# Kernel tuning notes

Hardware: AMD Instinct MI355X
Metric: run time of the kernel (lower is better)

The kernel has to match this reference:

```python
import jax, jax.numpy as jnp
import numpy as np
import math

B, L, E, H, D = 2, 2048, 2048, 16, 128
LOGIT_SCALE_MAX = math.log(1.0 / 0.01)
EPS = 1e-6


def rms_norm(x, scale, eps=EPS):
    # UIOLayerNorm: no mean subtraction, no bias, fp32 internals
    x32 = x.astype(jnp.float32)
    ms = jnp.mean(x32 * x32, axis=-1, keepdims=True)
    return (scale * (x32 * jax.lax.rsqrt(ms + eps)).astype(x.dtype)).astype(x.dtype)


def apply_rotary(x, rope):
    # x: [b, l, h, d]; rope: [b, l, d] interpreted as (cos, sin) interleaved pairs
    b, l, h, d = x.shape
    xr = x.astype(jnp.float32).reshape(b, l, h, d // 2, 2)
    rc = rope.astype(jnp.float32).reshape(b, l, 1, d // 2, 2)
    out = jnp.stack(
        [xr[..., 0] * rc[..., 0] - xr[..., 1] * rc[..., 1],
         xr[..., 1] * rc[..., 0] + xr[..., 0] * rc[..., 1]], axis=-1)
    return out.reshape(b, l, h, d).astype(x.dtype)


def l2_normalize(x, eps=1e-12):
    # matches F.normalize(dim=-1): x / max(||x||, eps)
    n = jnp.sqrt(jnp.sum(x * x, axis=-1, keepdims=True))
    return x / jnp.maximum(n, eps)


def setup_inputs() -> dict:
    key = jax.random.key(0)
    ks = jax.random.split(key, 12)
    scale = 1.0 / math.sqrt(E)
    return {
        "inputs_q": jax.random.normal(ks[0], (B, L, E), jnp.float32),
        "inputs_kv": jax.random.normal(ks[1], (B, L, E), jnp.float32),
        "bias": jax.random.normal(ks[2], (1, 1, L, L), jnp.float32),
        "q_sinusoids": jax.random.uniform(ks[3], (B, L, D), jnp.float32, -1.0, 1.0),
        "k_sinusoids": jax.random.uniform(ks[4], (B, L, D), jnp.float32, -1.0, 1.0),
        "Wq": jax.random.normal(ks[5], (E, E), jnp.float32) * scale,
        "Wk": jax.random.normal(ks[6], (E, E), jnp.float32) * scale,
        "Wv": jax.random.normal(ks[7], (E, E), jnp.float32) * scale,
        "Wo": jax.random.normal(ks[8], (E, E), jnp.float32) * scale,
        "q_norm_scale": jnp.ones((D,), jnp.float32),
        "k_norm_scale": jnp.ones((D,), jnp.float32),
        "logit_scale": jnp.full((H,), math.log(10.0), jnp.float32),
    }


def reference(inputs_q, inputs_kv, bias, q_sinusoids, k_sinusoids,
              Wq, Wk, Wv, Wo, q_norm_scale, k_norm_scale, logit_scale):
    dtype = inputs_q.dtype
    b, ql, e = inputs_q.shape
    kl = inputs_kv.shape[1]
    # QKV projections (nn.Linear, no bias), split heads -> [b, len, h, d]
    q = (inputs_q @ Wq.T).reshape(b, ql, H, D)
    k = (inputs_kv @ Wk.T).reshape(b, kl, H, D)
    v = (inputs_kv @ Wv.T).reshape(b, kl, H, D)
    # qk_norm (UIO RMS norm over head_dim)
    q = rms_norm(q, q_norm_scale)
    k = rms_norm(k, k_norm_scale)
    # RoPE
    q = apply_rotary(q, q_sinusoids)
    k = apply_rotary(k, k_sinusoids)
    # float32_logits
    q32 = q.astype(jnp.float32)
    k32 = k.astype(jnp.float32)
    # scaled cosine attention: L2-normalize q,k; learned per-head logit scale
    scores = jnp.einsum("bqhd,bkhd->bhqk", l2_normalize(q32), l2_normalize(k32))
    ls = jnp.exp(jnp.minimum(logit_scale, LOGIT_SCALE_MAX))
    scores = scores * ls[None, :, None, None]
    scores = scores + bias.astype(scores.dtype)
    attn = jax.nn.softmax(scores, axis=-1).astype(dtype)
    out = jnp.einsum("bhqk,bkhd->bqhd", attn, v)
    out = out.reshape(b, ql, e)
    return out @ Wo.T
```

## Files before the change

kernel.cpp:

```cpp
#include <hip/hip_runtime.h>
#include <hip/hip_bf16.h>

#define B_ 2
#define L_ 2048
#define E_ 2048
#define H_ 16
#define D_ 128
#define M_ (B_*L_)
#define LOGIT_SCALE_MAX_ 4.6051701859880914f
#define LOG2E_ 1.44269504088896f

typedef __bf16 bf16_t;
typedef __bf16 bf16x2 __attribute__((ext_vector_type(2)));
typedef __bf16 bf16x4 __attribute__((ext_vector_type(4)));
typedef __bf16 bf16x8 __attribute__((ext_vector_type(8)));
typedef float f32x4 __attribute__((ext_vector_type(4)));
typedef float f32x16 __attribute__((ext_vector_type(16)));

#define KSB(p, r, cb) ((p) * 32768 + (r) * 256 + ((cb) ^ (((r) & 7) << 4)))
#define VSB(p, r, cb) ((p) * 32768 + 16384 + (r) * 128 + ((cb) ^ (((r) & 7) << 4)))

#define NW_ 4194304L
#define NX_ 8388608L

__global__ void cvt_all_k(const float* __restrict__ xq, const float* __restrict__ xkv,
                          const float* __restrict__ bias,
                          const float* __restrict__ wq, const float* __restrict__ wk,
                          const float* __restrict__ wv, const float* __restrict__ wo,
                          bf16_t* __restrict__ ws) {
    const long NW4 = NW_ / 4, NX4 = NX_ / 4;
    long i4 = (long)blockIdx.x * 256 + threadIdx.x;
    const float* src; long off; float scale = 1.0f;
    if (i4 < 4 * NW4) {
        long r = i4 / NW4;
        src = (r == 0) ? wq : (r == 1) ? wk : (r == 2) ? wv : wo;
        off = i4 - r * NW4;
    } else if (i4 < 5 * NW4) {
        src = bias; off = i4 - 4 * NW4; scale = LOG2E_;
    } else if (i4 < 5 * NW4 + NX4) {
        src = xq; off = i4 - 5 * NW4;
    } else {
        src = xkv; off = i4 - 5 * NW4 - NX4;
    }
    float4 v = ((const float4*)src)[off];
    bf16x4 o = { (bf16_t)(v.x * scale), (bf16_t)(v.y * scale),
                 (bf16_t)(v.z * scale), (bf16_t)(v.w * scale) };
    ((bf16x4*)ws)[i4] = o;
}

template<typename OutT, int GROUPS>
__global__ __launch_bounds__(512, 2) void gemm256(
    const bf16_t* __restrict__ A0g, const bf16_t* __restrict__ A1g,
    const bf16_t* __restrict__ W0, OutT* __restrict__ C0) {
    __shared__ __align__(16) unsigned char smem[131072];
    const int tid = threadIdx.x;
    const int wid = tid >> 6, lane = tid & 63;
    const int fr = lane & 15, fq = lane >> 4;
    const int wm = wid >> 2, wn = wid & 3;
    int bid = blockIdx.x;
    { int cpx = (int)gridDim.x >> 3; bid = (bid & 7) * cpx + (bid >> 3); }
    const int g = (GROUPS > 1) ? (bid >> 7) : 0;
    const int wg = (GROUPS > 1) ? (bid & 127) : bid;
    const int bm = wg >> 3, bn = wg & 7;
    const long arow0 = (long)bm * 256;
    const long brow0 = (long)bn * 256;
    const bf16_t* Ab = ((GROUPS > 1 && g > 0) ? A1g : A0g) + arow0 * E_;
    const bf16_t* Wb = W0 + (long)g * (long)E_ * E_ + brow0 * E_;

    f32x4 acc[8][4] = {};

    const int srow = tid >> 2;
    const int sc16 = tid & 3;
    auto STG = [&](const bf16_t* base, unsigned matOff, int h, unsigned bufb, int kt) {
        #pragma unroll
        for (int kk = 0; kk < 2; ++kk) {
            int col = kk * 32 + ((sc16 ^ ((srow >> 1) & 3)) * 8);
            __builtin_amdgcn_global_load_lds(
                (const __attribute__((address_space(1))) void*)(base + (long)(h * 128 + srow) * E_ + kt + col),
                (__attribute__((address_space(3))) void*)(smem + bufb + matOff + h * 16384u + kk * 8192u + tid * 16), 16, 0, 0);
        }
    };
    auto LDA = [&](unsigned pb, int kk, int mi) -> bf16x8 {
        int r = wm * 128 + mi * 16 + fr;
        int lr = r & 127;
        return *(const bf16x8*)(smem + pb + (unsigned)(r >> 7) * 16384u + kk * 8192u + lr * 64 + ((fq ^ ((lr >> 1) & 3)) << 4));
    };
    auto LDB = [&](unsigned pb, int kk, int ni) -> bf16x8 {
        int r = wn * 64 + ni * 16 + fr;
        int lr = r & 127;
        return *(const bf16x8*)(smem + pb + 32768u + (unsigned)(r >> 7) * 16384u + kk * 8192u + lr * 64 + ((fq ^ ((lr >> 1) & 3)) << 4));
    };

    STG(Ab, 0u,     0, 0u, 0); STG(Ab, 0u,     1, 0u, 0);
    STG(Wb, 32768u, 0, 0u, 0); STG(Wb, 32768u, 1, 0u, 0);
    STG(Wb, 32768u, 0, 65536u, 64); STG(Wb, 32768u, 1, 65536u, 64);
    asm volatile("s_waitcnt vmcnt(4)" ::: "memory");
    __builtin_amdgcn_s_barrier();

    bf16x8 bq[2][4];
    #pragma unroll 2
    for (int t = 0; t < 32; ++t) {
        const unsigned pb = (unsigned)(t & 1) * 65536u;
        const unsigned sbA = 65536u - pb;
        const int ktA = ((t + 1) & 31) * 64;
        const int ktB = ((t + 2) & 31) * 64;
        bf16x8 a[2][2];
        #pragma unroll
        for (int kk = 0; kk < 2; ++kk) {
            a[kk][0] = LDA(pb, kk, 0); a[kk][1] = LDA(pb, kk, 1);
            #pragma unroll
            for (int ni = 0; ni < 4; ++ni) bq[kk][ni] = LDB(pb, kk, ni);
        }
        STG(Ab, 0u, 0, sbA, ktA);
        __builtin_amdgcn_s_barrier();
        asm volatile("s_waitcnt lgkmcnt(0)" ::: "memory");
        __builtin_amdgcn_sched_barrier(0);
        __builtin_amdgcn_s_setprio(1);
        #pragma unroll
        for (int kk = 0; kk < 2; ++kk)
            #pragma unroll
            for (int ni = 0; ni < 4; ++ni) {
                acc[0][ni] = __builtin_amdgcn_mfma_f32_16x16x32_bf16(a[kk][0], bq[kk][ni], acc[0][ni], 0, 0, 0);
                acc[1][ni] = __builtin_amdgcn_mfma_f32_16x16x32_bf16(a[kk][1], bq[kk][ni], acc[1][ni], 0, 0, 0);
            }
        __builtin_amdgcn_s_setprio(0);
        __builtin_amdgcn_s_barrier();
        #pragma unroll
        for (int kk = 0; kk < 2; ++kk) { a[kk][0] = LDA(pb, kk, 2); a[kk][1] = LDA(pb, kk, 3); }
        STG(Ab, 0u, 1, sbA, ktA);
        __builtin_amdgcn_s_barrier();
        asm volatile("s_waitcnt lgkmcnt(0)" ::: "memory");
        __builtin_amdgcn_sched_barrier(0);
        __builtin_amdgcn_s_setprio(1);
        #pragma unroll
        for (int kk = 0; kk < 2; ++kk)
            #pragma unroll
            for (int ni = 0; ni < 4; ++ni) {
                acc[2][ni] = __builtin_amdgcn_mfma_f32_16x16x32_bf16(a[kk][0], bq[kk][ni], acc[2][ni], 0, 0, 0);
                acc[3][ni] = __builtin_amdgcn_mfma_f32_16x16x32_bf16(a[kk][1], bq[kk][ni], acc[3][ni], 0, 0, 0);
            }
        __builtin_amdgcn_s_setprio(0);
        __builtin_amdgcn_s_barrier();
        #pragma unroll
        for (int kk = 0; kk < 2; ++kk) { a[kk][0] = LDA(pb, kk, 4); a[kk][1] = LDA(pb, kk, 5); }
        STG(Wb, 32768u, 0, pb, ktB);
        __builtin_amdgcn_s_barrier();
        asm volatile("s_waitcnt lgkmcnt(0)" ::: "memory");
        __builtin_amdgcn_sched_barrier(0);
        __builtin_amdgcn_s_setprio(1);
        #pragma unroll
        for (int kk = 0; kk < 2; ++kk)
            #pragma unroll
            for (int ni = 0; ni < 4; ++ni) {
                acc[4][ni] = __builtin_amdgcn_mfma_f32_16x16x32_bf16(a[kk][0], bq[kk][ni], acc[4][ni], 0, 0, 0);
                acc[5][ni] = __builtin_amdgcn_mfma_f32_16x16x32_bf16(a[kk][1], bq[kk][ni], acc[5][ni], 0, 0, 0);
            }
        __builtin_amdgcn_s_setprio(0);
        __builtin_amdgcn_s_barrier();
        #pragma unroll
        for (int kk = 0; kk < 2; ++kk) { a[kk][0] = LDA(pb, kk, 6); a[kk][1] = LDA(pb, kk, 7); }
        STG(Wb, 32768u, 1, pb, ktB);
        asm volatile("s_waitcnt vmcnt(4)" ::: "memory");
        __builtin_amdgcn_s_barrier();
        asm volatile("s_waitcnt lgkmcnt(0)" ::: "memory");
        __builtin_amdgcn_sched_barrier(0);
        __builtin_amdgcn_s_setprio(1);
        #pragma unroll
        for (int kk = 0; kk < 2; ++kk)
            #pragma unroll
            for (int ni = 0; ni < 4; ++ni) {
                acc[6][ni] = __builtin_amdgcn_mfma_f32_16x16x32_bf16(a[kk][0], bq[kk][ni], acc[6][ni], 0, 0, 0);
                acc[7][ni] = __builtin_amdgcn_mfma_f32_16x16x32_bf16(a[kk][1], bq[kk][ni], acc[7][ni], 0, 0, 0);
            }
        __builtin_amdgcn_s_setprio(0);
        __builtin_amdgcn_s_barrier();
    }
    asm volatile("s_waitcnt vmcnt(0)" ::: "memory");
    OutT* Cg = C0 + (long)g * M_ * E_;
    #pragma unroll
    for (int mi = 0; mi < 8; ++mi) {
        #pragma unroll
        for (int i = 0; i < 4; ++i) {
            long row = arow0 + wm * 128 + mi * 16 + fq * 4 + i;
            OutT* crow = Cg + row * E_ + brow0 + wn * 64 + fr;
            #pragma unroll
            for (int ni = 0; ni < 4; ++ni)
                crow[ni * 16] = (OutT)acc[mi][ni][i];
        }
    }
}

template<typename OutT>
__global__ __launch_bounds__(512, 2) void gemm8o(
    const bf16_t* __restrict__ A0g, const bf16_t* __restrict__ W0, OutT* __restrict__ C0) {
    __shared__ __align__(16) unsigned char smem[98304];
    const int tid = threadIdx.x;
    const int wid = tid >> 6, lane = tid & 63;
    const int fr = lane & 15, fq = lane >> 4;
    const int wm = wid & 3, wn = wid >> 2;
    int bid = blockIdx.x;
    { int cpx = (int)gridDim.x >> 3; bid = (bid & 7) * cpx + (bid >> 3); }
    const int bm = bid >> 4, bn = bid & 15;
    const long arow0 = (long)bm * 256;
    const long brow0 = (long)bn * 128;
    const bf16_t* Ab = A0g + arow0 * E_;
    const bf16_t* Wb = W0 + brow0 * E_;

    f32x4 acc[4][4] = {};

    auto STAGE_A = [&](unsigned sbase, int kk, int j, int ktn_) {
        int row = j * 128 + (tid >> 2);
        int c16 = tid & 3;
        int col = kk * 32 + ((c16 ^ ((row >> 1) & 3)) * 8);
        __builtin_amdgcn_global_load_lds(
            (const __attribute__((address_space(1))) void*)(Ab + (long)row * E_ + ktn_ + col),
            (__attribute__((address_space(3))) void*)(smem + sbase + kk * 16384 + j * 8192 + tid * 16), 16, 0, 0);
    };
    auto STAGE_B = [&](unsigned sbase, int kk, int ktn_) {
        int row = tid >> 2;
        int c16 = tid & 3;
        int col = kk * 32 + ((c16 ^ ((row >> 1) & 3)) * 8);
        __builtin_amdgcn_global_load_lds(
            (const __attribute__((address_space(1))) void*)(Wb + (long)row * E_ + ktn_ + col),
            (__attribute__((address_space(3))) void*)(smem + sbase + 32768 + kk * 8192 + tid * 16), 16, 0, 0);
    };
    auto LDA = [&](unsigned pbase, int kk, int mi) -> bf16x8 {
        int row = wm * 64 + mi * 16 + fr;
        return *(const bf16x8*)(smem + pbase + kk * 16384 + row * 64 + ((fq ^ ((row >> 1) & 3)) << 4));
    };
    auto LDB = [&](unsigned pbase, int kk, int ni) -> bf16x8 {
        int row = wn * 64 + ni * 16 + fr;
        return *(const bf16x8*)(smem + pbase + 32768 + kk * 8192 + row * 64 + ((fq ^ ((row >> 1) & 3)) << 4));
    };

    STAGE_A(0, 0, 0, 0); STAGE_A(0, 0, 1, 0); STAGE_B(0, 0, 0);
    STAGE_A(0, 1, 0, 0); STAGE_A(0, 1, 1, 0); STAGE_B(0, 1, 0);
    asm volatile("s_waitcnt vmcnt(0)" ::: "memory");
    __builtin_amdgcn_s_barrier();

    #pragma unroll 2
    for (int t = 0; t < 32; ++t) {
        const unsigned pb = (unsigned)(t & 1) * 49152u;
        const unsigned sb = 49152u - pb;
        const int ktn = (t < 31) ? (t + 1) * 64 : 0;
        bf16x8 bq[4], a0, a1;
        a0 = LDA(pb, 0, 0); a1 = LDA(pb, 0, 1);
        bq[0] = LDB(pb, 0, 0); bq[1] = LDB(pb, 0, 1); bq[2] = LDB(pb, 0, 2); bq[3] = LDB(pb, 0, 3);
        STAGE_A(sb, 0, 0, ktn); STAGE_A(sb, 0, 1, ktn);
        __builtin_amdgcn_s_barrier();
        asm volatile("s_waitcnt lgkmcnt(0)" ::: "memory");
        __builtin_amdgcn_sched_barrier(0);
        __builtin_amdgcn_s_setprio(1);
        #pragma unroll
        for (int ni = 0; ni < 4; ++ni) {
            acc[0][ni] = __builtin_amdgcn_mfma_f32_16x16x32_bf16(a0, bq[ni], acc[0][ni], 0, 0, 0);
            acc[1][ni] = __builtin_amdgcn_mfma_f32_16x16x32_bf16(a1, bq[ni], acc[1][ni], 0, 0, 0);
        }
        __builtin_amdgcn_s_setprio(0);
        __builtin_amdgcn_s_barrier();
        a0 = LDA(pb, 0, 2); a1 = LDA(pb, 0, 3);
        STAGE_B(sb, 0, ktn);
        asm volatile("s_waitcnt vmcnt(3)" ::: "memory");
        __builtin_amdgcn_s_barrier();
        asm volatile("s_waitcnt lgkmcnt(0)" ::: "memory");
        __builtin_amdgcn_sched_barrier(0);
        __builtin_amdgcn_s_setprio(1);
        #pragma unroll
        for (int ni = 0; ni < 4; ++ni) {
            acc[2][ni] = __builtin_amdgcn_mfma_f32_16x16x32_bf16(a0, bq[ni], acc[2][ni], 0, 0, 0);
            acc[3][ni] = __builtin_amdgcn_mfma_f32_16x16x32_bf16(a1, bq[ni], acc[3][ni], 0, 0, 0);
        }
        __builtin_amdgcn_s_setprio(0);
        __builtin_amdgcn_s_barrier();
        a0 = LDA(pb, 1, 0); a1 = LDA(pb, 1, 1);
        bq[0] = LDB(pb, 1, 0); bq[1] = LDB(pb, 1, 1); bq[2] = LDB(pb, 1, 2); bq[3] = LDB(pb, 1, 3);
        STAGE_A(sb, 1, 0, ktn); STAGE_A(sb, 1, 1, ktn);
        __builtin_amdgcn_s_barrier();
        asm volatile("s_waitcnt lgkmcnt(0)" ::: "memory");
        __builtin_amdgcn_sched_barrier(0);
        __builtin_amdgcn_s_setprio(1);
        #pragma unroll
        for (int ni = 0; ni < 4; ++ni) {
            acc[0][ni] = __builtin_amdgcn_mfma_f32_16x16x32_bf16(a0, bq[ni], acc[0][ni], 0, 0, 0);
            acc[1][ni] = __builtin_amdgcn_mfma_f32_16x16x32_bf16(a1, bq[ni], acc[1][ni], 0, 0, 0);
        }
        __builtin_amdgcn_s_setprio(0);
        __builtin_amdgcn_s_barrier();
        a0 = LDA(pb, 1, 2); a1 = LDA(pb, 1, 3);
        STAGE_B(sb, 1, ktn);
        asm volatile("s_waitcnt vmcnt(3)" ::: "memory");
        __builtin_amdgcn_s_barrier();
        asm volatile("s_waitcnt lgkmcnt(0)" ::: "memory");
        __builtin_amdgcn_sched_barrier(0);
        __builtin_amdgcn_s_setprio(1);
        #pragma unroll
        for (int ni = 0; ni < 4; ++ni) {
            acc[2][ni] = __builtin_amdgcn_mfma_f32_16x16x32_bf16(a0, bq[ni], acc[2][ni], 0, 0, 0);
            acc[3][ni] = __builtin_amdgcn_mfma_f32_16x16x32_bf16(a1, bq[ni], acc[3][ni], 0, 0, 0);
        }
        __builtin_amdgcn_s_setprio(0);
        __builtin_amdgcn_s_barrier();
    }
    #pragma unroll
    for (int mi = 0; mi < 4; ++mi) {
        #pragma unroll
        for (int i = 0; i < 4; ++i) {
            long row = arow0 + wm * 64 + mi * 16 + fq * 4 + i;
            OutT* crow = C0 + row * E_ + brow0 + wn * 64 + fr;
            #pragma unroll
            for (int ni = 0; ni < 4; ++ni)
                crow[ni * 16] = (OutT)acc[mi][ni][i];
        }
    }
}

__global__ __launch_bounds__(256) void post_tv_k(
    const bf16_t* __restrict__ Pq, const bf16_t* __restrict__ Pk,
    const bf16_t* __restrict__ Vp,
    const float* __restrict__ qsins, const float* __restrict__ ksins,
    const float* __restrict__ qnscale, const float* __restrict__ knscale,
    bf16_t* __restrict__ outq, bf16_t* __restrict__ outk, bf16_t* __restrict__ Vt) {
    __shared__ bf16_t t[64 * 64];
    if (blockIdx.x < 32768) {
        const int wid = threadIdx.x >> 6, lane = threadIdx.x & 63;
        const int half = blockIdx.x >> 14;
        const long g = (long)(blockIdx.x & 16383) * 4 + wid;
        const bf16_t* P = half ? Pk : Pq;
        const float* sins = half ? ksins : qsins;
        const float* nscale = half ? knscale : qnscale;
        bf16_t* out = half ? outk : outq;
        const int h = (int)(g % H_);
        const long bl = g / H_;
        const int b = (int)(bl / L_), l = (int)(bl % L_);
        bf16x2 xv = *(const bf16x2*)(P + g * D_ + lane * 2);
        float x0 = (float)xv[0], x1 = (float)xv[1];
        float ss = x0 * x0 + x1 * x1;
        #pragma unroll
        for (int m = 1; m < 64; m <<= 1) ss += __shfl_xor(ss, m);
        float r = rsqrtf(ss * (1.0f / 128.0f) + 1e-6f);
        float y0 = x0 * r * nscale[lane * 2];
        float y1 = x1 * r * nscale[lane * 2 + 1];
        float2 cs = *(const float2*)(sins + bl * D_ + lane * 2);
        float z0 = y0 * cs.x - y1 * cs.y;
        float z1 = y1 * cs.x + y0 * cs.y;
        float n2 = z0 * z0 + z1 * z1;
        #pragma unroll
        for (int m = 1; m < 64; m <<= 1) n2 += __shfl_xor(n2, m);
        float inv = 1.0f / fmaxf(sqrtf(n2), 1e-12f);
        bf16x2 o = { (bf16_t)(z0 * inv), (bf16_t)(z1 * inv) };
        *(bf16x2*)(out + (((long)b * H_ + h) * L_ + l) * D_ + lane * 2) = o;
    } else {
        const int idx = blockIdx.x - 32768;
        const int lb = idx & 31;
        const int db = (idx >> 5) & 1;
        const int bh = idx >> 6;
        const int b = bh >> 4, h = bh & 15;
        const bf16_t* src = Vp + ((long)(b * L_ + lb * 64) * H_ + h) * D_ + db * 64;
        #pragma unroll
        for (int it = 0; it < 2; ++it) {
            int i = it * 256 + threadIdx.x;
            int r = i >> 3, c8 = i & 7;
            bf16x8 v = *(const bf16x8*)(src + (long)r * H_ * D_ + c8 * 8);
            *(bf16x8*)&t[r * 64 + (c8 ^ (r >> 3)) * 8] = v;
        }
        __syncthreads();
        bf16_t* dst = Vt + ((long)(b * H_ + h) * D_ + db * 64) * L_ + lb * 64;
        #pragma unroll
        for (int it = 0; it < 2; ++it) {
            int i = it * 256 + threadIdx.x;
            int d = i >> 3, l8 = i & 7;
            bf16x8 o;
            #pragma unroll
            for (int j = 0; j < 8; ++j) {
                int l = l8 * 8 + j;
                o[j] = t[l * 64 + ((d >> 3) ^ l8) * 8 + (d & 7)];
            }
            *(bf16x8*)(dst + (long)d * L_ + l8 * 8) = o;
        }
    }
}

__global__ __launch_bounds__(256, 2) void attn_k(
    const bf16_t* __restrict__ Qn, const bf16_t* __restrict__ Kn,
    const bf16_t* __restrict__ Vt, const bf16_t* __restrict__ biasb,
    const float* __restrict__ lsg, bf16_t* __restrict__ AO) {
    __shared__ __align__(16) unsigned char smem[65536];
    const int tid = threadIdx.x;
    const int w = tid >> 6, lane = tid & 63;
    const int lane31 = lane & 31, hi = lane >> 5;
    const int qb = blockIdx.x, bh = blockIdx.y;
    const int b = bh >> 4, h = bh & 15;
    const float lsc2 = __expf(fminf(lsg[h], LOGIT_SCALE_MAX_)) * LOG2E_;
    const int qr0 = qb * 128;
    const int qloc = w * 32 + lane31;
    const bf16_t* qrow  = Qn + (((long)b * H_ + h) * L_ + qr0 + qloc) * D_;
    const bf16_t* kbase = Kn + (((long)b * H_ + h) * L_) * D_;
    const bf16_t* vtbase = Vt + ((long)(b * H_ + h) * D_) * L_;
    const bf16_t* brow  = biasb + (long)(qr0 + qloc) * L_;

    const int ksr = tid >> 4, ksc = (tid & 15) * 8;
    const int vsr = tid >> 3, vsc = (tid & 7) * 8;

    bf16x8 qreg[8];
    #pragma unroll
    for (int kk = 0; kk < 8; ++kk)
        qreg[kk] = *(const bf16x8*)(qrow + kk * 16 + 8 * hi);

    f32x16 oacc[4] = {};
    float l_ = 0.f;

    bf16x8 kreg[4], vreg[4];
    #pragma unroll
    for (int it = 0; it < 4; ++it) {
        kreg[it] = *(const bf16x8*)(kbase + (long)(it * 16 + ksr) * D_ + ksc);
        vreg[it] = *(const bf16x8*)(vtbase + (long)(it * 32 + vsr) * L_ + vsc);
    }
    #pragma unroll
    for (int it = 0; it < 4; ++it) {
        *(bf16x8*)(smem + KSB(0, it * 16 + ksr, ksc * 2)) = kreg[it];
        *(bf16x8*)(smem + VSB(0, it * 32 + vsr, vsc * 2)) = vreg[it];
    }
    int p = 0;

    for (int kt = 0; kt < L_; kt += 64) {
        __syncthreads();
        const int ktn = (kt + 64 < L_) ? kt + 64 : 0;
        #pragma unroll
        for (int it = 0; it < 4; ++it) {
            kreg[it] = *(const bf16x8*)(kbase + (long)(ktn + it * 16 + ksr) * D_ + ksc);
            vreg[it] = *(const bf16x8*)(vtbase + (long)(it * 32 + vsr) * L_ + ktn + vsc);
        }
        bf16x4 bb[2][4];
        #pragma unroll
        for (int f = 0; f < 2; ++f)
            #pragma unroll
            for (int rr = 0; rr < 4; ++rr)
                bb[f][rr] = *(const bf16x4*)(brow + kt + f * 32 + rr * 8 + 4 * hi);
        f32x16 sacc[2] = {};
        __builtin_amdgcn_s_setprio(1);
        #pragma unroll
        for (int kk = 0; kk < 8; ++kk) {
            bf16x8 ak0 = *(const bf16x8*)(smem + KSB(p, lane31,      kk * 32 + 16 * hi));
            bf16x8 ak1 = *(const bf16x8*)(smem + KSB(p, 32 + lane31, kk * 32 + 16 * hi));
            sacc[0] = __builtin_amdgcn_mfma_f32_32x32x16_bf16(ak0, qreg[kk], sacc[0], 0, 0, 0);
            sacc[1] = __builtin_amdgcn_mfma_f32_32x32x16_bf16(ak1, qreg[kk], sacc[1], 0, 0, 0);
        }
        __builtin_amdgcn_s_setprio(0);
        float ps = 0.f;
        unsigned int wv[2][4][2];
        #pragma unroll
        for (int f = 0; f < 2; ++f)
            #pragma unroll
            for (int rr = 0; rr < 4; ++rr)
                #pragma unroll
                for (int wi = 0; wi < 2; ++wi) {
                    float pa = __builtin_amdgcn_exp2f(sacc[f][rr * 4 + wi * 2]     * lsc2 + (float)bb[f][rr][wi * 2]);
                    float pc = __builtin_amdgcn_exp2f(sacc[f][rr * 4 + wi * 2 + 1] * lsc2 + (float)bb[f][rr][wi * 2 + 1]);
                    ps += pa + pc;
                    bf16x2 t = { (bf16_t)pa, (bf16_t)pc };
                    wv[f][rr][wi] = __builtin_bit_cast(unsigned int, t);
                }
        ps += __shfl_xor(ps, 32);
        l_ += ps;
        bf16x8 pb_[4];
        #pragma unroll
        for (int kk = 0; kk < 4; ++kk) {
            const int f = kk >> 1;
            const int a2 = (kk & 1) * 2;
            unsigned int A0 = wv[f][a2][0],     A1 = wv[f][a2][1];
            unsigned int B0 = wv[f][a2 + 1][0], B1 = wv[f][a2 + 1][1];
            unsigned int own0  = hi ? B0 : A0;
            unsigned int own1  = hi ? B1 : A1;
            unsigned int send0 = hi ? A0 : B0;
            unsigned int send1 = hi ? A1 : B1;
            unsigned int recv0 = __shfl_xor(send0, 32);
            unsigned int recv1 = __shfl_xor(send1, 32);
            uint4 uu;
            uu.x = hi ? recv0 : own0;
            uu.y = hi ? recv1 : own1;
            uu.z = hi ? own0  : recv0;
            uu.w = hi ? own1  : recv1;
            pb_[kk] = __builtin_bit_cast(bf16x8, uu);
        }
        __builtin_amdgcn_s_setprio(1);
        #pragma unroll
        for (int df = 0; df < 4; ++df)
            #pragma unroll
            for (int kk = 0; kk < 4; ++kk) {
                bf16x8 av = *(const bf16x8*)(smem + VSB(p, df * 32 + lane31, kk * 32 + 16 * hi));
                oacc[df] = __builtin_amdgcn_mfma_f32_32x32x16_bf16(av, pb_[kk], oacc[df], 0, 0, 0);
            }
        __builtin_amdgcn_s_setprio(0);
        if (kt + 64 < L_) {
            #pragma unroll
            for (int it = 0; it < 4; ++it) {
                *(bf16x8*)(smem + KSB(p ^ 1, it * 16 + ksr, ksc * 2)) = kreg[it];
                *(bf16x8*)(smem + VSB(p ^ 1, it * 32 + vsr, vsc * 2)) = vreg[it];
            }
        }
        p ^= 1;
    }
    __syncthreads();
    float inv = 1.0f / l_;
    #pragma unroll
    for (int df = 0; df < 4; ++df)
        #pragma unroll
        for (int rg = 0; rg < 16; ++rg) {
            int d = df * 32 + (rg & 3) + 8 * (rg >> 2) + 4 * hi;
            *(bf16_t*)(smem + qloc * 264 + d * 2) = (bf16_t)(oacc[df][rg] * inv);
        }
    __syncthreads();
    #pragma unroll
    for (int it = 0; it < 8; ++it) {
        int idx = it * 256 + tid;
        int row = idx >> 4, c = idx & 15;
        bf16x8 v = *(const bf16x8*)(smem + row * 264 + c * 16);
        *(bf16x8*)(AO + ((long)b * L_ + qr0 + row) * E_ + h * D_ + c * 8) = v;
    }
}

extern "C" void kernel_launch(void* const* d_in, const int* in_sizes, int n_in,
                              void* d_out, int out_size, void* d_ws, size_t ws_size,
                              hipStream_t stream) {
    const float* inputs_q  = (const float*)d_in[0];
    const float* inputs_kv = (const float*)d_in[1];
    const float* bias      = (const float*)d_in[2];
    const float* q_sin     = (const float*)d_in[3];
    const float* k_sin     = (const float*)d_in[4];
    const float* Wq        = (const float*)d_in[5];
    const float* Wk        = (const float*)d_in[6];
    const float* Wv        = (const float*)d_in[7];
    const float* Wo        = (const float*)d_in[8];
    const float* qns       = (const float*)d_in[9];
    const float* kns       = (const float*)d_in[10];
    const float* lsg       = (const float*)d_in[11];

    bf16_t* ws = (bf16_t*)d_ws;
    const long NW = NW_;
    const long NX = NX_;
    bf16_t* Wq_b   = ws;
    bf16_t* Wo_b   = ws + 3 * NW;
    bf16_t* bias_b = ws + 4 * NW;
    bf16_t* Xq     = bias_b + NW;
    bf16_t* Xkv    = Xq + NX;
    bf16_t* Qp     = Xkv + NX;
    bf16_t* Kp     = Qp + NX;
    bf16_t* Vp     = Kp + NX;
    bf16_t* Qn = Xq;
    bf16_t* Kn = Xkv;
    bf16_t* AO = Qp;
    bf16_t* Vtr = Kp;
    if (ws_size < (size_t)(5 * NW + 5 * NX) * 2) return;

    {
        long n4 = (5 * NW + 2 * NX) / 4;
        cvt_all_k<<<dim3((unsigned)(n4 / 256)), dim3(256), 0, stream>>>(
            inputs_q, inputs_kv, bias, Wq, Wk, Wv, Wo, ws);
    }

    gemm256<bf16_t, 3><<<dim3(384), dim3(512), 0, stream>>>(Xq, Xkv, Wq_b, Qp);

    post_tv_k<<<dim3(34816), dim3(256), 0, stream>>>(
        Qp, Kp, Vp, q_sin, k_sin, qns, kns, Qn, Kn, Vtr);

    attn_k<<<dim3(L_ / 128, B_ * H_), dim3(256), 0, stream>>>(Qn, Kn, Vtr, bias_b, lsg, AO);

    gemm8o<float><<<dim3(256), dim3(512), 0, stream>>>(AO, Wo_b, (float*)d_out);
}
```

Measured before the change: 311.1 us.

## Split QKV GEMM into mixed full and half-height tiles to balance waves

The QKV projection GEMM now launches 512 blocks. The first 256 compute full 256x256 tiles, and the last 128 tiles are split into two 128-row halves each, so the 256-CU device gets a better-balanced second wave instead of a partial one. The output projection GEMM reuses the half-tile path of the same kernel in place of the separate gemm8o kernel, so it now uses 128x256 tiles rather than 256x128. Half tiles reuse the W tile less per block, which adds global and L2 traffic.

```diff
diff --git a/kernel.cpp b/kernel.cpp
--- a/kernel.cpp
+++ b/kernel.cpp
@@ -48,8 +48,8 @@
     ((bf16x4*)ws)[i4] = o;
 }
 
-template<typename OutT, int GROUPS>
-__global__ __launch_bounds__(512, 2) void gemm256(
+template<typename OutT, int GROUPS, int FULLB>
+__global__ __launch_bounds__(512, 2) void gemm_mix(
     const bf16_t* __restrict__ A0g, const bf16_t* __restrict__ A1g,
     const bf16_t* __restrict__ W0, OutT* __restrict__ C0) {
     __shared__ __align__(16) unsigned char smem[131072];
@@ -57,20 +57,29 @@
     const int wid = tid >> 6, lane = tid & 63;
     const int fr = lane & 15, fq = lane >> 4;
     const int wm = wid >> 2, wn = wid & 3;
-    int bid = blockIdx.x;
-    { int cpx = (int)gridDim.x >> 3; bid = (bid & 7) * cpx + (bid >> 3); }
-    const int g = (GROUPS > 1) ? (bid >> 7) : 0;
-    const int wg = (GROUPS > 1) ? (bid & 127) : bid;
-    const int bm = wg >> 3, bn = wg & 7;
-    const long arow0 = (long)bm * 256;
+    int slot, hsel, isfull;
+    {
+        int bid = blockIdx.x;
+        if (FULLB > 0 && bid < FULLB) {
+            slot = (bid & 7) * (FULLB >> 3) + (bid >> 3);
+            hsel = 0; isfull = 1;
+        } else {
+            const int n = (int)gridDim.x - FULLB;
+            int sub = bid - FULLB;
+            int s = (sub & 7) * (n >> 3) + (sub >> 3);
+            slot = FULLB + (s >> 1); hsel = s & 1; isfull = 0;
+        }
+    }
+    const int g = slot >> 7;
+    const int r0 = slot & 127;
+    const int bm = r0 >> 3, bn = r0 & 7;
+    const long arow0 = (long)bm * 256 + (long)hsel * 128;
     const long brow0 = (long)bn * 256;
     const bf16_t* Ab = ((GROUPS > 1 && g > 0) ? A1g : A0g) + arow0 * E_;
     const bf16_t* Wb = W0 + (long)g * (long)E_ * E_ + brow0 * E_;
-
-    f32x4 acc[8][4] = {};
-
     const int srow = tid >> 2;
     const int sc16 = tid & 3;
+
     auto STG = [&](const bf16_t* base, unsigned matOff, int h, unsigned bufb, int kt) {
         #pragma unroll
         for (int kk = 0; kk < 2; ++kk) {
@@ -80,8 +89,7 @@
                 (__attribute__((address_space(3))) void*)(smem + bufb + matOff + h * 16384u + kk * 8192u + tid * 16), 16, 0, 0);
         }
     };
-    auto LDA = [&](unsigned pb, int kk, int mi) -> bf16x8 {
-        int r = wm * 128 + mi * 16 + fr;
+    auto LDA = [&](unsigned pb, int kk, int r) -> bf16x8 {
         int lr = r & 127;
         return *(const bf16x8*)(smem + pb + (unsigned)(r >> 7) * 16384u + kk * 8192u + lr * 64 + ((fq ^ ((lr >> 1) & 3)) << 4));
     };
@@ -91,226 +99,201 @@
         return *(const bf16x8*)(smem + pb + 32768u + (unsigned)(r >> 7) * 16384u + kk * 8192u + lr * 64 + ((fq ^ ((lr >> 1) & 3)) << 4));
     };
 
-    STG(Ab, 0u,     0, 0u, 0); STG(Ab, 0u,     1, 0u, 0);
-    STG(Wb, 32768u, 0, 0u, 0); STG(Wb, 32768u, 1, 0u, 0);
-    STG(Wb, 32768u, 0, 65536u, 64); STG(Wb, 32768u, 1, 65536u, 64);
-    asm volatile("s_waitcnt vmcnt(4)" ::: "memory");
-    __builtin_amdgcn_s_barrier();
-
-    bf16x8 bq[2][4];
-    #pragma unroll 2
-    for (int t = 0; t < 32; ++t) {
-        const unsigned pb = (unsigned)(t & 1) * 65536u;
-        const unsigned sbA = 65536u - pb;
-        const int ktA = ((t + 1) & 31) * 64;
-        const int ktB = ((t + 2) & 31) * 64;
-        bf16x8 a[2][2];
-        #pragma unroll
-        for (int kk = 0; kk < 2; ++kk) {
-            a[kk][0] = LDA(pb, kk, 0); a[kk][1] = LDA(pb, kk, 1);
-            #pragma unroll
-            for (int ni = 0; ni < 4; ++ni) bq[kk][ni] = LDB(pb, kk, ni);
-        }
-        STG(Ab, 0u, 0, sbA, ktA);
-        __builtin_amdgcn_s_barrier();
-        asm volatile("s_waitcnt lgkmcnt(0)" ::: "memory");
-        __builtin_amdgcn_sched_barrier(0);
-        __builtin_amdgcn_s_setprio(1);
-        #pragma unroll
-        for (int kk = 0; kk < 2; ++kk)
-            #pragma unroll
-            for (int ni = 0; ni < 4; ++ni) {
-                acc[0][ni] = __builtin_amdgcn_mfma_f32_16x16x32_bf16(a[kk][0], bq[kk][ni], acc[0][ni], 0, 0, 0);
-                acc[1][ni] = __builtin_amdgcn_mfma_f32_16x16x32_bf16(a[kk][1], bq[kk][ni], acc[1][ni], 0, 0, 0);
-            }
-        __builtin_amdgcn_s_setprio(0);
-        __builtin_amdgcn_s_barrier();
-        #pragma unroll
-        for (int kk = 0; kk < 2; ++kk) { a[kk][0] = LDA(pb, kk, 2); a[kk][1] = LDA(pb, kk, 3); }
-        STG(Ab, 0u, 1, sbA, ktA);
-        __builtin_amdgcn_s_barrier();
-        asm volatile("s_waitcnt lgkmcnt(0)" ::: "memory");
-        __builtin_amdgcn_sched_barrier(0);
-        __builtin_amdgcn_s_setprio(1);
-        #pragma unroll
-        for (int kk = 0; kk < 2; ++kk)
-            #pragma unroll
-            for (int ni = 0; ni < 4; ++ni) {
-                acc[2][ni] = __builtin_amdgcn_mfma_f32_16x16x32_bf16(a[kk][0], bq[kk][ni], acc[2][ni], 0, 0, 0);
-                acc[3][ni] = __builtin_amdgcn_mfma_f32_16x16x32_bf16(a[kk][1], bq[kk][ni], acc[3][ni], 0, 0, 0);
-            }
-        __builtin_amdgcn_s_setprio(0);
-        __builtin_amdgcn_s_barrier();
-        #pragma unroll
-        for (int kk = 0; kk < 2; ++kk) { a[kk][0] = LDA(pb, kk, 4); a[kk][1] = LDA(pb, kk, 5); }
-        STG(Wb, 32768u, 0, pb, ktB);
-        __builtin_amdgcn_s_barrier();
-        asm volatile("s_waitcnt lgkmcnt(0)" ::: "memory");
-        __builtin_amdgcn_sched_barrier(0);
-        __builtin_amdgcn_s_setprio(1);
-        #pragma unroll
-        for (int kk = 0; kk < 2; ++kk)
-            #pragma unroll
-            for (int ni = 0; ni < 4; ++ni) {
-                acc[4][ni] = __builtin_amdgcn_mfma_f32_16x16x32_bf16(a[kk][0], bq[kk][ni], acc[4][ni], 0, 0, 0);
-                acc[5][ni] = __builtin_amdgcn_mfma_f32_16x16x32_bf16(a[kk][1], bq[kk][ni], acc[5][ni], 0, 0, 0);
-            }
-        __builtin_amdgcn_s_setprio(0);
-        __builtin_amdgcn_s_barrier();
-        #pragma unroll
-        for (int kk = 0; kk < 2; ++kk) { a[kk][0] = LDA(pb, kk, 6); a[kk][1] = LDA(pb, kk, 7); }
-        STG(Wb, 32768u, 1, pb, ktB);
+    if (FULLB > 0 && isfull) {
+        f32x4 acc[8][4] = {};
+        STG(Ab, 0u,     0, 0u, 0); STG(Ab, 0u,     1, 0u, 0);
+        STG(Wb, 32768u, 0, 0u, 0); STG(Wb, 32768u, 1, 0u, 0);
+        STG(Wb, 32768u, 0, 65536u, 64); STG(Wb, 32768u, 1, 65536u, 64);
         asm volatile("s_waitcnt vmcnt(4)" ::: "memory");
         __builtin_amdgcn_s_barrier();
-        asm volatile("s_waitcnt lgkmcnt(0)" ::: "memory");
-        __builtin_amdgcn_sched_barrier(0);
-        __builtin_amdgcn_s_setprio(1);
-        #pragma unroll
-        for (int kk = 0; kk < 2; ++kk)
-            #pragma unroll
-            for (int ni = 0; ni < 4; ++ni) {
-                acc[6][ni] = __builtin_amdgcn_mfma_f32_16x16x32_bf16(a[kk][0], bq[kk][ni], acc[6][ni], 0, 0, 0);
-                acc[7][ni] = __builtin_amdgcn_mfma_f32_16x16x32_bf16(a[kk][1], bq[kk][ni], acc[7][ni], 0, 0, 0);
-            }
-        __builtin_amdgcn_s_setprio(0);
+        bf16x8 bq[2][4];
+        #pragma unroll 2
+        for (int t = 0; t < 32; ++t) {
+            const unsigned pb = (unsigned)(t & 1) * 65536u;
+            const unsigned sbA = 65536u - pb;
+            const int ktA = ((t + 1) & 31) * 64;
+            const int ktB = ((t + 2) & 31) * 64;
+            bf16x8 a[2][2];
+            #pragma unroll
+            for (int kk = 0; kk < 2; ++kk) {
+                a[kk][0] = LDA(pb, kk, wm * 128 + 0 * 16 + fr);
+                a[kk][1] = LDA(pb, kk, wm * 128 + 1 * 16 + fr);
+                #pragma unroll
+                for (int ni = 0; ni < 4; ++ni) bq[kk][ni] = LDB(pb, kk, ni);
+            }
+            STG(Ab, 0u, 0, sbA, ktA);
+            __builtin_amdgcn_s_barrier();
+            asm volatile("s_waitcnt lgkmcnt(0)" ::: "memory");
+            __builtin_amdgcn_sched_barrier(0);
+            __builtin_amdgcn_s_setprio(1);
+            #pragma unroll
+            for (int kk = 0; kk < 2; ++kk)
+                #pragma unroll
+                for (int ni = 0; ni < 4; ++ni) {
+                    acc[0][ni] = __builtin_amdgcn_mfma_f32_16x16x32_bf16(a[kk][0], bq[kk][ni], acc[0][ni], 0, 0, 0);
+                    acc[1][ni] = __builtin_amdgcn_mfma_f32_16x16x32_bf16(a[kk][1], bq[kk][ni], acc[1][ni], 0, 0, 0);
+                }
+            __builtin_amdgcn_s_setprio(0);
+            __builtin_amdgcn_s_barrier();
+            #pragma unroll
+            for (int kk = 0; kk < 2; ++kk) {
+                a[kk][0] = LDA(pb, kk, wm * 128 + 2 * 16 + fr);
+                a[kk][1] = LDA(pb, kk, wm * 128 + 3 * 16 + fr);
+            }
+            STG(Ab, 0u, 1, sbA, ktA);
+            __builtin_amdgcn_s_barrier();
+            asm volatile("s_waitcnt lgkmcnt(0)" ::: "memory");
+            __builtin_amdgcn_sched_barrier(0);
+            __builtin_amdgcn_s_setprio(1);
+            #pragma unroll
+            for (int kk = 0; kk < 2; ++kk)
+                #pragma unroll
+                for (int ni = 0; ni < 4; ++ni) {
+                    acc[2][ni] = __builtin_amdgcn_mfma_f32_16x16x32_bf16(a[kk][0], bq[kk][ni], acc[2][ni], 0, 0, 0);
+                    acc[3][ni] = __builtin_amdgcn_mfma_f32_16x16x32_bf16(a[kk][1], bq[kk][ni], acc[3][ni], 0, 0, 0);
+                }
+            __builtin_amdgcn_s_setprio(0);
+            __builtin_amdgcn_s_barrier();
+            #pragma unroll
+            for (int kk = 0; kk < 2; ++kk) {
+                a[kk][0] = LDA(pb, kk, wm * 128 + 4 * 16 + fr);
+                a[kk][1] = LDA(pb, kk, wm * 128 + 5 * 16 + fr);
+            }
+            STG(Wb, 32768u, 0, pb, ktB);
+            __builtin_amdgcn_s_barrier();
+            asm volatile("s_waitcnt lgkmcnt(0)" ::: "memory");
+            __builtin_amdgcn_sched_barrier(0);
+            __builtin_amdgcn_s_setprio(1);
+            #pragma unroll
+            for (int kk = 0; kk < 2; ++kk)
+                #pragma unroll
+                for (int ni = 0; ni < 4; ++ni) {
+                    acc[4][ni] = __builtin_amdgcn_mfma_f32_16x16x32_bf16(a[kk][0], bq[kk][ni], acc[4][ni], 0, 0, 0);
+                    acc[5][ni] = __builtin_amdgcn_mfma_f32_16x16x32_bf16(a[kk][1], bq[kk][ni], acc[5][ni], 0, 0, 0);
+                }
+            __builtin_amdgcn_s_setprio(0);
+            __builtin_amdgcn_s_barrier();
+            #pragma unroll
+            for (int kk = 0; kk < 2; ++kk) {
+                a[kk][0] = LDA(pb, kk, wm * 128 + 6 * 16 + fr);
+                a[kk][1] = LDA(pb, kk, wm * 128 + 7 * 16 + fr);
+            }
+            STG(Wb, 32768u, 1, pb, ktB);
+            asm volatile("s_waitcnt vmcnt(4)" ::: "memory");
+            __builtin_amdgcn_s_barrier();
+            asm volatile("s_waitcnt lgkmcnt(0)" ::: "memory");
+            __builtin_amdgcn_sched_barrier(0);
+            __builtin_amdgcn_s_setprio(1);
+            #pragma unroll
+            for (int kk = 0; kk < 2; ++kk)
+                #pragma unroll
+                for (int ni = 0; ni < 4; ++ni) {
+                    acc[6][ni] = __builtin_amdgcn_mfma_f32_16x16x32_bf16(a[kk][0], bq[kk][ni], acc[6][ni], 0, 0, 0);
+                    acc[7][ni] = __builtin_amdgcn_mfma_f32_16x16x32_bf16(a[kk][1], bq[kk][ni], acc[7][ni], 0, 0, 0);
+                }
+            __builtin_amdgcn_s_setprio(0);
+            __builtin_amdgcn_s_barrier();
+        }
+        asm volatile("s_waitcnt vmcnt(0)" ::: "memory");
+        OutT* Cg = C0 + (long)g * M_ * E_;
+        #pragma unroll
+        for (int mi = 0; mi < 8; ++mi)
+            #pragma unroll
+            for (int i = 0; i < 4; ++i) {
+                long row = arow0 + wm * 128 + mi * 16 + fq * 4 + i;
+                OutT* crow = Cg + row * E_ + brow0 + wn * 64 + fr;
+                #pragma unroll
+                for (int ni = 0; ni < 4; ++ni)
+                    crow[ni * 16] = (OutT)acc[mi][ni][i];
+            }
+    } else {
+        f32x4 acc[4][4] = {};
+        STG(Ab, 0u,     0, 0u, 0);
+        STG(Wb, 32768u, 0, 0u, 0); STG(Wb, 32768u, 1, 0u, 0);
+        STG(Wb, 32768u, 0, 65536u, 64); STG(Wb, 32768u, 1, 65536u, 64);
+        asm volatile("s_waitcnt vmcnt(4)" ::: "memory");
         __builtin_amdgcn_s_barrier();
-    }
-    asm volatile("s_waitcnt vmcnt(0)" ::: "memory");
-    OutT* Cg = C0 + (long)g * M_ * E_;
-    #pragma unroll
-    for (int mi = 0; mi < 8; ++mi) {
-        #pragma unroll
-        for (int i = 0; i < 4; ++i) {
-            long row = arow0 + wm * 128 + mi * 16 + fq * 4 + i;
-            OutT* crow = Cg + row * E_ + brow0 + wn * 64 + fr;
-            #pragma unroll
-            for (int ni = 0; ni < 4; ++ni)
-                crow[ni * 16] = (OutT)acc[mi][ni][i];
-        }
-    }
-}
-
-template<typename OutT>
-__global__ __launch_bounds__(512, 2) void gemm8o(
-    const bf16_t* __restrict__ A0g, const bf16_t* __restrict__ W0, OutT* __restrict__ C0) {
-    __shared__ __align__(16) unsigned char smem[98304];
-    const int tid = threadIdx.x;
-    const int wid = tid >> 6, lane = tid & 63;
-    const int fr = lane & 15, fq = lane >> 4;
-    const int wm = wid & 3, wn = wid >> 2;
-    int bid = blockIdx.x;
-    { int cpx = (int)gridDim.x >> 3; bid = (bid & 7) * cpx + (bid >> 3); }
-    const int bm = bid >> 4, bn = bid & 15;
-    const long arow0 = (long)bm * 256;
-    const long brow0 = (long)bn * 128;
-    const bf16_t* Ab = A0g + arow0 * E_;
-    const bf16_t* Wb = W0 + brow0 * E_;
-
-    f32x4 acc[4][4] = {};
-
-    auto STAGE_A = [&](unsigned sbase, int kk, int j, int ktn_) {
-        int row = j * 128 + (tid >> 2);
-        int c16 = tid & 3;
-        int col = kk * 32 + ((c16 ^ ((row >> 1) & 3)) * 8);
-        __builtin_amdgcn_global_load_lds(
-            (const __attribute__((address_space(1))) void*)(Ab + (long)row * E_ + ktn_ + col),
-            (__attribute__((address_space(3))) void*)(smem + sbase + kk * 16384 + j * 8192 + tid * 16), 16, 0, 0);
-    };
-    auto STAGE_B = [&](unsigned sbase, int kk, int ktn_) {
-        int row = tid >> 2;
-        int c16 = tid & 3;
-        int col = kk * 32 + ((c16 ^ ((row >> 1) & 3)) * 8);
-        __builtin_amdgcn_global_load_lds(
-            (const __attribute__((address_space(1))) void*)(Wb + (long)row * E_ + ktn_ + col),
-            (__attribute__((address_space(3))) void*)(smem + sbase + 32768 + kk * 8192 + tid * 16), 16, 0, 0);
-    };
-    auto LDA = [&](unsigned pbase, int kk, int mi) -> bf16x8 {
-        int row = wm * 64 + mi * 16 + fr;
-        return *(const bf16x8*)(smem + pbase + kk * 16384 + row * 64 + ((fq ^ ((row >> 1) & 3)) << 4));
-    };
-    auto LDB = [&](unsigned pbase, int kk, int ni) -> bf16x8 {
-        int row = wn * 64 + ni * 16 + fr;
-        return *(const bf16x8*)(smem + pbase + 32768 + kk * 8192 + row * 64 + ((fq ^ ((row >> 1) & 3)) << 4));
-    };
-
-    STAGE_A(0, 0, 0, 0); STAGE_A(0, 0, 1, 0); STAGE_B(0, 0, 0);
-    STAGE_A(0, 1, 0, 0); STAGE_A(0, 1, 1, 0); STAGE_B(0, 1, 0);
-    asm volatile("s_waitcnt vmcnt(0)" ::: "memory");
-    __builtin_amdgcn_s_barrier();
-
-    #pragma unroll 2
-    for (int t = 0; t < 32; ++t) {
-        const unsigned pb = (unsigned)(t & 1) * 49152u;
-        const unsigned sb = 49152u - pb;
-        const int ktn = (t < 31) ? (t + 1) * 64 : 0;
-        bf16x8 bq[4], a0, a1;
-        a0 = LDA(pb, 0, 0); a1 = LDA(pb, 0, 1);
-        bq[0] = LDB(pb, 0, 0); bq[1] = LDB(pb, 0, 1); bq[2] = LDB(pb, 0, 2); bq[3] = LDB(pb, 0, 3);
-        STAGE_A(sb, 0, 0, ktn); STAGE_A(sb, 0, 1, ktn);
-        __builtin_amdgcn_s_barrier();
-        asm volatile("s_waitcnt lgkmcnt(0)" ::: "memory");
-        __builtin_amdgcn_sched_barrier(0);
-        __builtin_amdgcn_s_setprio(1);
-        #pragma unroll
-        for (int ni = 0; ni < 4; ++ni) {
-            acc[0][ni] = __builtin_amdgcn_mfma_f32_16x16x32_bf16(a0, bq[ni], acc[0][ni], 0, 0, 0);
-            acc[1][ni] = __builtin_amdgcn_mfma_f32_16x16x32_bf16(a1, bq[ni], acc[1][ni], 0, 0, 0);
-        }
-        __builtin_amdgcn_s_setprio(0);
-        __builtin_amdgcn_s_barrier();
-        a0 = LDA(pb, 0, 2); a1 = LDA(pb, 0, 3);
-        STAGE_B(sb, 0, ktn);
-        asm volatile("s_waitcnt vmcnt(3)" ::: "memory");
-        __builtin_amdgcn_s_barrier();
-        asm volatile("s_waitcnt lgkmcnt(0)" ::: "memory");
-        __builtin_amdgcn_sched_barrier(0);
-        __builtin_amdgcn_s_setprio(1);
-        #pragma unroll
-        for (int ni = 0; ni < 4; ++ni) {
-            acc[2][ni] = __builtin_amdgcn_mfma_f32_16x16x32_bf16(a0, bq[ni], acc[2][ni], 0, 0, 0);
-            acc[3][ni] = __builtin_amdgcn_mfma_f32_16x16x32_bf16(a1, bq[ni], acc[3][ni], 0, 0, 0);
-        }
-        __builtin_amdgcn_s_setprio(0);
-        __builtin_amdgcn_s_barrier();
-        a0 = LDA(pb, 1, 0); a1 = LDA(pb, 1, 1);
-        bq[0] = LDB(pb, 1, 0); bq[1] = LDB(pb, 1, 1); bq[2] = LDB(pb, 1, 2); bq[3] = LDB(pb, 1, 3);
-        STAGE_A(sb, 1, 0, ktn); STAGE_A(sb, 1, 1, ktn);
-        __builtin_amdgcn_s_barrier();
-        asm volatile("s_waitcnt lgkmcnt(0)" ::: "memory");
-        __builtin_amdgcn_sched_barrier(0);
-        __builtin_amdgcn_s_setprio(1);
-        #pragma unroll
-        for (int ni = 0; ni < 4; ++ni) {
-            acc[0][ni] = __builtin_amdgcn_mfma_f32_16x16x32_bf16(a0, bq[ni], acc[0][ni], 0, 0, 0);
-            acc[1][ni] = __builtin_amdgcn_mfma_f32_16x16x32_bf16(a1, bq[ni], acc[1][ni], 0, 0, 0);
-        }
-        __builtin_amdgcn_s_setprio(0);
-        __builtin_amdgcn_s_barrier();
-        a0 = LDA(pb, 1, 2); a1 = LDA(pb, 1, 3);
-        STAGE_B(sb, 1, ktn);
-        asm volatile("s_waitcnt vmcnt(3)" ::: "memory");
-        __builtin_amdgcn_s_barrier();
-        asm volatile("s_waitcnt lgkmcnt(0)" ::: "memory");
-        __builtin_amdgcn_sched_barrier(0);
-        __builtin_amdgcn_s_setprio(1);
-        #pragma unroll
-        for (int ni = 0; ni < 4; ++ni) {
-            acc[2][ni] = __builtin_amdgcn_mfma_f32_16x16x32_bf16(a0, bq[ni], acc[2][ni], 0, 0, 0);
-            acc[3][ni] = __builtin_amdgcn_mfma_f32_16x16x32_bf16(a1, bq[ni], acc[3][ni], 0, 0, 0);
-        }
-        __builtin_amdgcn_s_setprio(0);
-        __builtin_amdgcn_s_barrier();
-    }
-    #pragma unroll
-    for (int mi = 0; mi < 4; ++mi) {
-        #pragma unroll
-        for (int i = 0; i < 4; ++i) {
-            long row = arow0 + wm * 64 + mi * 16 + fq * 4 + i;
-            OutT* crow = C0 + row * E_ + brow0 + wn * 64 + fr;
-            #pragma unroll
-            for (int ni = 0; ni < 4; ++ni)
-                crow[ni * 16] = (OutT)acc[mi][ni][i];
-        }
+        bf16x8 bq[2][4];
+        #pragma unroll 2
+        for (int t = 0; t < 32; ++t) {
+            const unsigned pb = (unsigned)(t & 1) * 65536u;
+            const unsigned sbA = 65536u - pb;
+            const int ktA = ((t + 1) & 31) * 64;
+            const int ktB = ((t + 2) & 31) * 64;
+            bf16x8 a[2];
+            #pragma unroll
+            for (int kk = 0; kk < 2; ++kk) {
+                a[kk] = LDA(pb, kk, wm * 64 + 0 * 16 + fr);
+                #pragma unroll
+                for (int ni = 0; ni < 4; ++ni) bq[kk][ni] = LDB(pb, kk, ni);
+            }
+            STG(Ab, 0u, 0, sbA, ktA);
+            __builtin_amdgcn_s_barrier();
+            asm volatile("s_waitcnt lgkmcnt(0)" ::: "memory");
+            __builtin_amdgcn_sched_barrier(0);
+            __builtin_amdgcn_s_setprio(1);
+            #pragma unroll
+            for (int kk = 0; kk < 2; ++kk)
+                #pragma unroll
+                for (int ni = 0; ni < 4; ++ni)
+                    acc[0][ni] = __builtin_amdgcn_mfma_f32_16x16x32_bf16(a[kk], bq[kk][ni], acc[0][ni], 0, 0, 0);
+            __builtin_amdgcn_s_setprio(0);
+            __builtin_amdgcn_s_barrier();
+            #pragma unroll
+            for (int kk = 0; kk < 2; ++kk) a[kk] = LDA(pb, kk, wm * 64 + 1 * 16 + fr);
+            __builtin_amdgcn_s_barrier();
+            asm volatile("s_waitcnt lgkmcnt(0)" ::: "memory");
+            __builtin_amdgcn_sched_barrier(0);
+            __builtin_amdgcn_s_setprio(1);
+            #pragma unroll
+            for (int kk = 0; kk < 2; ++kk)
+                #pragma unroll
+                for (int ni = 0; ni < 4; ++ni)
+                    acc[1][ni] = __builtin_amdgcn_mfma_f32_16x16x32_bf16(a[kk], bq[kk][ni], acc[1][ni], 0, 0, 0);
+            __builtin_amdgcn_s_setprio(0);
+            __builtin_amdgcn_s_barrier();
+            #pragma unroll
+            for (int kk = 0; kk < 2; ++kk) a[kk] = LDA(pb, kk, wm * 64 + 2 * 16 + fr);
+            STG(Wb, 32768u, 0, pb, ktB);
+            __builtin_amdgcn_s_barrier();
+            asm volatile("s_waitcnt lgkmcnt(0)" ::: "memory");
+            __builtin_amdgcn_sched_barrier(0);
+            __builtin_amdgcn_s_setprio(1);
+            #pragma unroll
+            for (int kk = 0; kk < 2; ++kk)
+                #pragma unroll
+                for (int ni = 0; ni < 4; ++ni)
+                    acc[2][ni] = __builtin_amdgcn_mfma_f32_16x16x32_bf16(a[kk], bq[kk][ni], acc[2][ni], 0, 0, 0);
+            __builtin_amdgcn_s_setprio(0);
+            __builtin_amdgcn_s_barrier();
+            #pragma unroll
+            for (int kk = 0; kk < 2; ++kk) a[kk] = LDA(pb, kk, wm * 64 + 3 * 16 + fr);
+            STG(Wb, 32768u, 1, pb, ktB);
+            asm volatile("s_waitcnt vmcnt(4)" ::: "memory");
+            __builtin_amdgcn_s_barrier();
+            asm volatile("s_waitcnt lgkmcnt(0)" ::: "memory");
+            __builtin_amdgcn_sched_barrier(0);
+            __builtin_amdgcn_s_setprio(1);
+            #pragma unroll
+            for (int kk = 0; kk < 2; ++kk)
+                #pragma unroll
+                for (int ni = 0; ni < 4; ++ni)
+                    acc[3][ni] = __builtin_amdgcn_mfma_f32_16x16x32_bf16(a[kk], bq[kk][ni], acc[3][ni], 0, 0, 0);
+            __builtin_amdgcn_s_setprio(0);
+            __builtin_amdgcn_s_barrier();
+        }
+        asm volatile("s_waitcnt vmcnt(0)" ::: "memory");
+        OutT* Cg = C0 + (long)g * M_ * E_;
+        #pragma unroll
+        for (int mi = 0; mi < 4; ++mi)
+            #pragma unroll
+            for (int i = 0; i < 4; ++i) {
+                long row = arow0 + wm * 64 + mi * 16 + fq * 4 + i;
+                OutT* crow = Cg + row * E_ + brow0 + wn * 64 + fr;
+                #pragma unroll
+                for (int ni = 0; ni < 4; ++ni)
+                    crow[ni * 16] = (OutT)acc[mi][ni][i];
+            }
     }
 }
 
@@ -558,12 +541,12 @@
             inputs_q, inputs_kv, bias, Wq, Wk, Wv, Wo, ws);
     }
 
-    gemm256<bf16_t, 3><<<dim3(384), dim3(512), 0, stream>>>(Xq, Xkv, Wq_b, Qp);
+    gemm_mix<bf16_t, 3, 256><<<dim3(512), dim3(512), 0, stream>>>(Xq, Xkv, Wq_b, Qp);
 
     post_tv_k<<<dim3(34816), dim3(256), 0, stream>>>(
         Qp, Kp, Vp, q_sin, k_sin, qns, kns, Qn, Kn, Vtr);
 
     attn_k<<<dim3(L_ / 128, B_ * H_), dim3(256), 0, stream>>>(Qn, Kn, Vtr, bias_b, lsg, AO);
 
-    gemm8o<float><<<dim3(256), dim3(512), 0, stream>>>(AO, Wo_b, (float*)d_out);
+    gemm_mix<float, 1, 0><<<dim3(256), dim3(512), 0, stream>>>(AO, AO, Wo_b, (float*)d_out);
 }
```

Result: no change. 316.8 us, median of 2 (+1.8%).
